# Kernel optimization log

Measured on AMD Instinct MI355X. Metric: run time of the kernel, lower is better.

The kernel has to match this reference:

```python
import jax, jax.numpy as jnp
import numpy as np
from jax import lax


def _dense_image_warp(img, flow):
    # TFA semantics: out[b,i,j] = bilinear_sample(img[b], (i - flow[b,i,j,0], j - flow[b,i,j,1]))
    # floors clamped to [0, size-2]; alphas clamped to [0, 1].
    B, H, W, C = img.shape
    gy = jnp.arange(H, dtype=flow.dtype)[None, :, None]
    gx = jnp.arange(W, dtype=flow.dtype)[None, None, :]
    qy = gy - flow[..., 0]
    qx = gx - flow[..., 1]
    fy = jnp.clip(jnp.floor(qy), 0.0, H - 2)
    fx = jnp.clip(jnp.floor(qx), 0.0, W - 2)
    ay = jnp.clip(qy - fy, 0.0, 1.0)[..., None]
    ax = jnp.clip(qx - fx, 0.0, 1.0)[..., None]
    fy = fy.astype(jnp.int32)
    fx = fx.astype(jnp.int32)
    b = jnp.arange(B)[:, None, None]
    tl = img[b, fy, fx]
    tr = img[b, fy, fx + 1]
    bl = img[b, fy + 1, fx]
    br = img[b, fy + 1, fx + 1]
    top = tl + ax * (tr - tl)
    bot = bl + ax * (br - bl)
    return top + ay * (bot - top)


def _conv(x, w, b, act):
    y = lax.conv_general_dilated(x, w, (1, 1), 'SAME',
                                 dimension_numbers=('NHWC', 'HWIO', 'NHWC')) + b
    return jax.nn.relu(y) if act else y


def _predict(x, ws, bs):
    for i in range(4):
        x = _conv(x, ws[i], bs[i], True)
    return _conv(x, ws[4], bs[4], False)  # final 1x1 -> 2 channels, linear


def _upsample2x(x):
    B, H, W, C = x.shape
    return jax.image.resize(x, (B, 2 * H, 2 * W, C), method='bilinear')


# Conv stack dims: in=64 (concat of two 32-ch maps)
_KSHAPES = [(3, 3, 64, 32), (3, 3, 32, 64), (1, 1, 64, 64), (1, 1, 64, 16), (1, 1, 16, 2)]


def setup_inputs() -> dict:
    key = jax.random.key(0)
    ks = jax.random.split(key, 4 + 2 * len(_KSHAPES))
    B, H, W, C = 8, 256, 256, 32
    inp = {
        'input_1': jax.random.normal(ks[0], (B, H, W, C), jnp.float32),
        'input_2': jax.random.normal(ks[1], (B, H, W, C), jnp.float32),
        'flow_1_2': jax.random.normal(ks[2], (B, H, W, 2), jnp.float32) * 3.0,
        'flow_2_1': jax.random.normal(ks[3], (B, H, W, 2), jnp.float32) * 3.0,
    }
    for i, sh in enumerate(_KSHAPES):
        inp[f'w12_{i}'] = jax.random.normal(ks[4 + i], sh, jnp.float32) * 0.05
        inp[f'b12_{i}'] = jnp.zeros((sh[-1],), jnp.float32)
        inp[f'w21_{i}'] = jax.random.normal(ks[4 + len(_KSHAPES) + i], sh, jnp.float32) * 0.05
        inp[f'b21_{i}'] = jnp.zeros((sh[-1],), jnp.float32)
    return inp


def reference(input_1, input_2, flow_1_2, flow_2_1,
              w12_0, b12_0, w12_1, b12_1, w12_2, b12_2, w12_3, b12_3, w12_4, b12_4,
              w21_0, b21_0, w21_1, b21_1, w21_2, b21_2, w21_3, b21_3, w21_4, b21_4):
    ws12 = [w12_0, w12_1, w12_2, w12_3, w12_4]
    bs12 = [b12_0, b12_1, b12_2, b12_3, b12_4]
    ws21 = [w21_0, w21_1, w21_2, w21_3, w21_4]
    bs21 = [b21_0, b21_1, b21_2, b21_3, b21_4]

    # 1 -> 2 direction
    input_1_warped_1 = _dense_image_warp(input_1, flow_1_2)
    flow_change_1_2 = _predict(jnp.concatenate([input_2, input_1_warped_1], axis=3), ws12, bs12)
    flow_1_2_changed = flow_1_2 + flow_change_1_2
    input_1_warped_2 = _dense_image_warp(input_1, flow_1_2_changed)
    flow_1_2_up = _upsample2x(flow_1_2_changed)

    # 2 -> 1 direction
    input_2_warped_1 = _dense_image_warp(input_2, flow_2_1)
    flow_change_2_1 = _predict(jnp.concatenate([input_1, input_2_warped_1], axis=3), ws21, bs21)
    flow_2_1_changed = flow_2_1 + flow_change_2_1
    input_2_warped_2 = _dense_image_warp(input_2, flow_2_1_changed)
    flow_2_1_up = _upsample2x(flow_2_1_changed)

    return (input_1_warped_2, input_2_warped_2, flow_1_2_up, flow_2_1_up)
```

## Files before the change

### kernel.cpp

```cpp
#include <hip/hip_runtime.h>
#include <hip/hip_bf16.h>
#include <cstddef>

#define B_ 8
#define H_ 256
#define W_ 256

static constexpr int NPIX = B_ * H_ * W_;

typedef __attribute__((ext_vector_type(8))) short bf16x8;
typedef __attribute__((ext_vector_type(4))) float f32x4;

__device__ __forceinline__ float4 ld4(const float* p) { return *(const float4*)p; }

__device__ __forceinline__ short f2bf(float x) {
    unsigned u = __float_as_uint(x);
    unsigned r = (u + 0x7fffu + ((u >> 16) & 1u)) >> 16;
    return (short)r;
}

__global__ __launch_bounds__(256) void cvt_inputs_kernel(
    const float* __restrict__ in1, const float* __restrict__ in2,
    short* __restrict__ xb1, short* __restrict__ xb2)
{
    int t = blockIdx.x * 256 + threadIdx.x;
    const int N8 = NPIX * 32 / 8;
    const float* src = (t < N8) ? in1 : in2;
    short* dst = (t < N8) ? xb1 : xb2;
    int i = (t < N8) ? t : t - N8;
    float4 a = ld4(src + (size_t)i * 8);
    float4 b = ld4(src + (size_t)i * 8 + 4);
    bf16x8 r;
    r[0] = f2bf(a.x); r[1] = f2bf(a.y); r[2] = f2bf(a.z); r[3] = f2bf(a.w);
    r[4] = f2bf(b.x); r[5] = f2bf(b.y); r[6] = f2bf(b.z); r[7] = f2bf(b.w);
    *(bf16x8*)(dst + (size_t)i * 8) = r;
}

__global__ __launch_bounds__(256) void prep_weights_kernel(
    const float* __restrict__ w0a, const float* __restrict__ w1a,
    const float* __restrict__ w2a, const float* __restrict__ w3a,
    const float* __restrict__ w0b, const float* __restrict__ w1b,
    const float* __restrict__ w2b, const float* __restrict__ w3b,
    short* __restrict__ wt0, short* __restrict__ wt1)
{
    int t = blockIdx.x * 256 + threadIdx.x;
    if (t >= 2 * 5248) return;
    int dir = t / 5248;
    int r = t % 5248;
    const float* w0 = dir ? w0b : w0a;
    const float* w1 = dir ? w1b : w1a;
    const float* w2 = dir ? w2b : w2a;
    const float* w3 = dir ? w3b : w3a;
    short* wt = dir ? wt1 : wt0;
    bf16x8 v;
    if (r < 2304) {
        int l = r & 63, n = (r >> 6) & 1, c = (r >> 7) & 1, tp = r >> 8;
#pragma unroll
        for (int j = 0; j < 8; ++j) {
            int ci = c * 32 + 8 * (l >> 4) + j;
            int co = n * 16 + (l & 15);
            v[j] = f2bf(w0[(size_t)(tp * 64 + ci) * 32 + co]);
        }
    } else if (r < 4608) {
        int q = r - 2304;
        int l = q & 63, n = (q >> 6) & 3, tp = q >> 8;
#pragma unroll
        for (int j = 0; j < 8; ++j) {
            int ci = 8 * (l >> 4) + j;
            int co = n * 16 + (l & 15);
            v[j] = f2bf(w1[(size_t)(tp * 32 + ci) * 64 + co]);
        }
    } else if (r < 5120) {
        int q = r - 4608;
        int l = q & 63, n = (q >> 6) & 3, c = q >> 8;
#pragma unroll
        for (int j = 0; j < 8; ++j) {
            int k = 32 * c + 8 * (l >> 4) + j;
            int co = n * 16 + (l & 15);
            v[j] = f2bf(w2[(size_t)k * 64 + co]);
        }
    } else {
        int q = r - 5120;
        int l = q & 63, c = q >> 6;
#pragma unroll
        for (int j = 0; j < 8; ++j) {
            int k = 32 * c + 8 * (l >> 4) + j;
            v[j] = f2bf(w3[(size_t)k * 16 + (l & 15)]);
        }
    }
    *(bf16x8*)(wt + (size_t)r * 8) = v;
}

__global__ __launch_bounds__(256) void warp_bf16_kernel(
    const float* __restrict__ in1, const float* __restrict__ in2,
    const float* __restrict__ fl12, const float* __restrict__ fl21,
    short* __restrict__ wbf)
{
    int gid = blockIdx.x * 256 + threadIdx.x;
    int d   = (gid >= NPIX * 8);
    int g2  = gid - (d ? NPIX * 8 : 0);
    const float* img  = d ? in2 : in1;
    const float* flow = d ? fl21 : fl12;
    short* out = wbf + (size_t)d * NPIX * 32;

    int p   = g2 >> 3;
    int c4  = (g2 & 7) << 2;
    int b   = p >> 16;
    int i   = (p >> 8) & 255;
    int j   = p & 255;
    float2 f = *(const float2*)(flow + (size_t)p * 2);
    float qy = (float)i - f.x;
    float qx = (float)j - f.y;
    float fyf = fminf(fmaxf(floorf(qy), 0.0f), (float)(H_ - 2));
    float fxf = fminf(fmaxf(floorf(qx), 0.0f), (float)(W_ - 2));
    float ay = fminf(fmaxf(qy - fyf, 0.0f), 1.0f);
    float ax = fminf(fmaxf(qx - fxf, 0.0f), 1.0f);
    int fy = (int)fyf, fx = (int)fxf;
    const float* base = img + ((((size_t)b * H_ + fy) * W_ + fx) << 5) + c4;
    float4 tl = ld4(base);
    float4 tr = ld4(base + 32);
    float4 bl = ld4(base + W_ * 32);
    float4 br = ld4(base + W_ * 32 + 32);
    short4 r;
    { float t = tl.x + ax * (tr.x - tl.x); float u = bl.x + ax * (br.x - bl.x); r.x = f2bf(t + ay * (u - t)); }
    { float t = tl.y + ax * (tr.y - tl.y); float u = bl.y + ax * (br.y - bl.y); r.y = f2bf(t + ay * (u - t)); }
    { float t = tl.z + ax * (tr.z - tl.z); float u = bl.z + ax * (br.z - bl.z); r.z = f2bf(t + ay * (u - t)); }
    { float t = tl.w + ax * (tr.w - tl.w); float u = bl.w + ax * (br.w - bl.w); r.w = f2bf(t + ay * (u - t)); }
    *(short4*)(out + ((size_t)p << 5) + c4) = r;
}

__global__ __launch_bounds__(256) void warp_f32_kernel(
    const float* __restrict__ in1, const float* __restrict__ in2,
    const float* __restrict__ fcb, float* __restrict__ outf)
{
    int gid = blockIdx.x * 256 + threadIdx.x;
    int d   = (gid >= NPIX * 8);
    int g2  = gid - (d ? NPIX * 8 : 0);
    const float* img  = d ? in2 : in1;
    const float* flow = fcb + (size_t)d * NPIX * 2;
    float* out = outf + (size_t)d * NPIX * 32;

    int p   = g2 >> 3;
    int c4  = (g2 & 7) << 2;
    int b   = p >> 16;
    int i   = (p >> 8) & 255;
    int j   = p & 255;
    float2 f = *(const float2*)(flow + (size_t)p * 2);
    float qy = (float)i - f.x;
    float qx = (float)j - f.y;
    float fyf = fminf(fmaxf(floorf(qy), 0.0f), (float)(H_ - 2));
    float fxf = fminf(fmaxf(floorf(qx), 0.0f), (float)(W_ - 2));
    float ay = fminf(fmaxf(qy - fyf, 0.0f), 1.0f);
    float ax = fminf(fmaxf(qx - fxf, 0.0f), 1.0f);
    int fy = (int)fyf, fx = (int)fxf;
    const float* base = img + ((((size_t)b * H_ + fy) * W_ + fx) << 5) + c4;
    float4 tl = ld4(base);
    float4 tr = ld4(base + 32);
    float4 bl = ld4(base + W_ * 32);
    float4 br = ld4(base + W_ * 32 + 32);
    float4 r;
    { float t = tl.x + ax * (tr.x - tl.x); float u = bl.x + ax * (br.x - bl.x); r.x = t + ay * (u - t); }
    { float t = tl.y + ax * (tr.y - tl.y); float u = bl.y + ax * (br.y - bl.y); r.y = t + ay * (u - t); }
    { float t = tl.z + ax * (tr.z - tl.z); float u = bl.z + ax * (br.z - bl.z); r.z = t + ay * (u - t); }
    { float t = tl.w + ax * (tr.w - tl.w); float u = bl.w + ax * (br.w - bl.w); r.w = t + ay * (u - t); }
    *(float4*)(out + ((size_t)p << 5) + c4) = r;
}

__global__ __launch_bounds__(512) void conv0_mfma_kernel(
    const short* __restrict__ xb1, const short* __restrict__ xb2,
    const short* __restrict__ wbf,
    const short* __restrict__ wt0, const short* __restrict__ wt1,
    const float* __restrict__ b0a, const float* __restrict__ b0b,
    short* __restrict__ h0)
{
    __shared__ short swt[2304 * 8];
    int d   = blockIdx.x >> 11;
    int bid = blockIdx.x & 2047;
    const short* xoth = d ? xb1 : xb2;
    const short* xw   = wbf + (size_t)d * NPIX * 32;
    const short* wtab = d ? wt1 : wt0;
    const float* bias = d ? b0b : b0a;
    short* out = h0 + (size_t)d * NPIX * 32;

    int tid = threadIdx.x;
    for (int i = tid; i < 2304; i += 512)
        ((bf16x8*)swt)[i] = ((const bf16x8*)wtab)[i];
    __syncthreads();

    int wave = tid >> 6, lane = tid & 63;
    int l15 = lane & 15, g = lane >> 4;
    int prow = bid * 256;
    int y    = bid & 255;
    int t0   = prow + wave * 32;
    int xl0  = wave * 32 + l15;
    int xl1  = xl0 + 16;

    const short* a0p = xoth + ((size_t)(t0 + l15) << 5) + g * 8;
    const short* a1p = a0p + (16 << 5);
    const short* b0p = xw + ((size_t)(t0 + l15) << 5) + g * 8;
    const short* b1p = b0p + (16 << 5);
    const bf16x8* wfrag = (const bf16x8*)swt;

    float bv0 = bias[l15], bv1 = bias[16 + l15];
    f32x4 acc00 = {bv0, bv0, bv0, bv0};
    f32x4 acc01 = {bv1, bv1, bv1, bv1};
    f32x4 acc10 = {bv0, bv0, bv0, bv0};
    f32x4 acc11 = {bv1, bv1, bv1, bv1};
    const bf16x8 z8 = {0, 0, 0, 0, 0, 0, 0, 0};

#pragma unroll
    for (int dy = -1; dy <= 1; ++dy) {
        if ((unsigned)(y + dy) >= (unsigned)H_) continue;
#pragma unroll
        for (int dx = -1; dx <= 1; ++dx) {
            bool v0 = (unsigned)(xl0 + dx) < (unsigned)W_;
            bool v1 = (unsigned)(xl1 + dx) < (unsigned)W_;
            int off0 = (dy * W_ + (v0 ? dx : 0)) << 5;
            int off1 = (dy * W_ + (v1 ? dx : 0)) << 5;
            bf16x8 aA0 = *(const bf16x8*)(a0p + off0);
            bf16x8 aB0 = *(const bf16x8*)(b0p + off0);
            bf16x8 aA1 = *(const bf16x8*)(a1p + off1);
            bf16x8 aB1 = *(const bf16x8*)(b1p + off1);
            aA0 = v0 ? aA0 : z8;  aB0 = v0 ? aB0 : z8;
            aA1 = v1 ? aA1 : z8;  aB1 = v1 ? aB1 : z8;
            int t = (dy + 1) * 3 + (dx + 1);
            bf16x8 w0 = wfrag[(t * 4 + 0) * 64 + lane];
            bf16x8 w1 = wfrag[(t * 4 + 1) * 64 + lane];
            bf16x8 w2 = wfrag[(t * 4 + 2) * 64 + lane];
            bf16x8 w3 = wfrag[(t * 4 + 3) * 64 + lane];
            acc00 = __builtin_amdgcn_mfma_f32_16x16x32_bf16(aA0, w0, acc00, 0, 0, 0);
            acc01 = __builtin_amdgcn_mfma_f32_16x16x32_bf16(aA0, w1, acc01, 0, 0, 0);
            acc10 = __builtin_amdgcn_mfma_f32_16x16x32_bf16(aA1, w0, acc10, 0, 0, 0);
            acc11 = __builtin_amdgcn_mfma_f32_16x16x32_bf16(aA1, w1, acc11, 0, 0, 0);
            acc00 = __builtin_amdgcn_mfma_f32_16x16x32_bf16(aB0, w2, acc00, 0, 0, 0);
            acc01 = __builtin_amdgcn_mfma_f32_16x16x32_bf16(aB0, w3, acc01, 0, 0, 0);
            acc10 = __builtin_amdgcn_mfma_f32_16x16x32_bf16(aB1, w2, acc10, 0, 0, 0);
            acc11 = __builtin_amdgcn_mfma_f32_16x16x32_bf16(aB1, w3, acc11, 0, 0, 0);
        }
    }

#pragma unroll
    for (int r = 0; r < 4; ++r) {
        size_t r0 = (size_t)(t0 + g * 4 + r) << 5;
        size_t r1 = (size_t)(t0 + 16 + g * 4 + r) << 5;
        out[r0 + l15]      = f2bf(fmaxf(acc00[r], 0.f));
        out[r0 + 16 + l15] = f2bf(fmaxf(acc01[r], 0.f));
        out[r1 + l15]      = f2bf(fmaxf(acc10[r], 0.f));
        out[r1 + 16 + l15] = f2bf(fmaxf(acc11[r], 0.f));
    }
}

__global__ __launch_bounds__(512) void conv1_mfma_kernel(
    const short* __restrict__ h0,
    const short* __restrict__ wt0, const short* __restrict__ wt1,
    const float* __restrict__ b1a, const float* __restrict__ b1b,
    const float* __restrict__ b2a, const float* __restrict__ b2b,
    const float* __restrict__ b3a, const float* __restrict__ b3b,
    const float* __restrict__ w4a, const float* __restrict__ w4b,
    const float* __restrict__ b4a, const float* __restrict__ b4b,
    const float* __restrict__ fl12, const float* __restrict__ fl21,
    float* __restrict__ fcb)
{
    __shared__ short swt[2944 * 8];
    __shared__ __align__(16) short sx[8][2048];
    int d   = blockIdx.x >> 11;
    int bid = blockIdx.x & 2047;
    const short* hsrc = h0 + (size_t)d * NPIX * 32;
    const short* wtab = (d ? wt1 : wt0) + 2304 * 8;
    const float* b1 = d ? b1b : b1a;
    const float* b2 = d ? b2b : b2a;
    const float* b3 = d ? b3b : b3a;
    const float* w4 = d ? w4b : w4a;
    const float* b4 = d ? b4b : b4a;
    const float* flow = d ? fl21 : fl12;
    float* fc = fcb + (size_t)d * NPIX * 2;

    int tid = threadIdx.x;
    for (int i = tid; i < 2944; i += 512)
        ((bf16x8*)swt)[i] = ((const bf16x8*)wtab)[i];
    __syncthreads();

    int wave = tid >> 6, lane = tid & 63;
    int l15 = lane & 15, g = lane >> 4;
    int prow = bid * 256;
    int y    = bid & 255;
    int t0   = prow + wave * 32;
    int xl0  = wave * 32 + l15;
    int xl1  = xl0 + 16;

    const short* a0p = hsrc + ((size_t)(t0 + l15) << 5) + g * 8;
    const short* a1p = a0p + (16 << 5);
    const bf16x8* W1 = (const bf16x8*)swt;
    const bf16x8* W2 = (const bf16x8*)swt + 2304;
    const bf16x8* W3 = (const bf16x8*)swt + 2816;
    char* xb = (char*)&sx[wave][0];
    const bf16x8 z8 = {0, 0, 0, 0, 0, 0, 0, 0};

    f32x4 acc0[4], acc1[4];
#pragma unroll
    for (int n = 0; n < 4; ++n) {
        float b = b1[n * 16 + l15];
        acc0[n] = (f32x4){b, b, b, b};
        acc1[n] = (f32x4){b, b, b, b};
    }
#pragma unroll
    for (int dy = -1; dy <= 1; ++dy) {
        if ((unsigned)(y + dy) >= (unsigned)H_) continue;
#pragma unroll
        for (int dx = -1; dx <= 1; ++dx) {
            bool v0 = (unsigned)(xl0 + dx) < (unsigned)W_;
            bool v1 = (unsigned)(xl1 + dx) < (unsigned)W_;
            int off0 = (dy * W_ + (v0 ? dx : 0)) << 5;
            int off1 = (dy * W_ + (v1 ? dx : 0)) << 5;
            bf16x8 a0 = *(const bf16x8*)(a0p + off0);
            bf16x8 a1 = *(const bf16x8*)(a1p + off1);
            a0 = v0 ? a0 : z8;
            a1 = v1 ? a1 : z8;
            int t = (dy + 1) * 3 + (dx + 1);
#pragma unroll
            for (int n = 0; n < 4; ++n) {
                bf16x8 w = W1[(t * 4 + n) * 64 + lane];
                acc0[n] = __builtin_amdgcn_mfma_f32_16x16x32_bf16(a0, w, acc0[n], 0, 0, 0);
                acc1[n] = __builtin_amdgcn_mfma_f32_16x16x32_bf16(a1, w, acc1[n], 0, 0, 0);
            }
        }
    }
#pragma unroll
    for (int n = 0; n < 4; ++n)
#pragma unroll
        for (int r = 0; r < 4; ++r) {
            int row0 = g * 4 + r, ch = n * 16 + l15;
            int by0 = (row0 * 128 + ch * 2) ^ ((row0 & 7) << 4);
            int by1 = ((row0 + 16) * 128 + ch * 2) ^ ((row0 & 7) << 4);
            *(short*)(xb + by0) = f2bf(fmaxf(acc0[n][r], 0.f));
            *(short*)(xb + by1) = f2bf(fmaxf(acc1[n][r], 0.f));
        }

#pragma unroll
    for (int n = 0; n < 4; ++n) {
        float b = b2[n * 16 + l15];
        acc0[n] = (f32x4){b, b, b, b};
        acc1[n] = (f32x4){b, b, b, b};
    }
#pragma unroll
    for (int c = 0; c < 2; ++c) {
        int by0 = (l15 * 128 + (32 * c + 8 * g) * 2) ^ ((l15 & 7) << 4);
        int by1 = ((l15 + 16) * 128 + (32 * c + 8 * g) * 2) ^ ((l15 & 7) << 4);
        bf16x8 a0 = *(const bf16x8*)(xb + by0);
        bf16x8 a1 = *(const bf16x8*)(xb + by1);
#pragma unroll
        for (int n = 0; n < 4; ++n) {
            bf16x8 w = W2[(c * 4 + n) * 64 + lane];
            acc0[n] = __builtin_amdgcn_mfma_f32_16x16x32_bf16(a0, w, acc0[n], 0, 0, 0);
            acc1[n] = __builtin_amdgcn_mfma_f32_16x16x32_bf16(a1, w, acc1[n], 0, 0, 0);
        }
    }
#pragma unroll
    for (int n = 0; n < 4; ++n)
#pragma unroll
        for (int r = 0; r < 4; ++r) {
            int row0 = g * 4 + r, ch = n * 16 + l15;
            int by0 = (row0 * 128 + ch * 2) ^ ((row0 & 7) << 4);
            int by1 = ((row0 + 16) * 128 + ch * 2) ^ ((row0 & 7) << 4);
            *(short*)(xb + by0) = f2bf(fmaxf(acc0[n][r], 0.f));
            *(short*)(xb + by1) = f2bf(fmaxf(acc1[n][r], 0.f));
        }

    float b3v = b3[l15];
    f32x4 acc3a = {b3v, b3v, b3v, b3v};
    f32x4 acc3b = {b3v, b3v, b3v, b3v};
#pragma unroll
    for (int c = 0; c < 2; ++c) {
        int by0 = (l15 * 128 + (32 * c + 8 * g) * 2) ^ ((l15 & 7) << 4);
        int by1 = ((l15 + 16) * 128 + (32 * c + 8 * g) * 2) ^ ((l15 & 7) << 4);
        bf16x8 a0 = *(const bf16x8*)(xb + by0);
        bf16x8 a1 = *(const bf16x8*)(xb + by1);
        bf16x8 w = W3[c * 64 + lane];
        acc3a = __builtin_amdgcn_mfma_f32_16x16x32_bf16(a0, w, acc3a, 0, 0, 0);
        acc3b = __builtin_amdgcn_mfma_f32_16x16x32_bf16(a1, w, acc3b, 0, 0, 0);
    }

    float w40 = w4[l15 * 2 + 0], w41 = w4[l15 * 2 + 1];
    float bb0 = b4[0], bb1 = b4[1];
#pragma unroll
    for (int tt = 0; tt < 2; ++tt) {
        f32x4 a3 = tt ? acc3b : acc3a;
#pragma unroll
        for (int r = 0; r < 4; ++r) {
            float v = fmaxf(a3[r], 0.f);
            float s0 = v * w40, s1 = v * w41;
#pragma unroll
            for (int m = 1; m < 16; m <<= 1) {
                s0 += __shfl_xor(s0, m);
                s1 += __shfl_xor(s1, m);
            }
            if (l15 == 0) {
                int pr = t0 + tt * 16 + g * 4 + r;
                float2 fl = *(const float2*)(flow + (size_t)pr * 2);
                float2 o; o.x = fl.x + bb0 + s0; o.y = fl.y + bb1 + s1;
                *(float2*)(fc + (size_t)pr * 2) = o;
            }
        }
    }
}

__global__ __launch_bounds__(256) void upsample_kernel(
    const float* __restrict__ fcb, float* __restrict__ outup)
{
    int gid = blockIdx.x * 256 + threadIdx.x;
    const int NUP = B_ * 512 * 512;
    int d  = (gid >= NUP);
    int g2 = gid - (d ? NUP : 0);
    const float* fc = fcb + (size_t)d * NPIX * 2;
    float* out = outup + (size_t)d * NUP * 2;

    int b  = g2 >> 18;
    int oy = (g2 >> 9) & 511;
    int ox = g2 & 511;
    float iy = 0.5f * (float)oy - 0.25f;
    float ix = 0.5f * (float)ox - 0.25f;
    float y0f = floorf(iy), x0f = floorf(ix);
    float wy = iy - y0f, wx = ix - x0f;
    int y0 = min(max((int)y0f, 0), H_ - 1);
    int y1 = min(max((int)y0f + 1, 0), H_ - 1);
    int x0 = min(max((int)x0f, 0), W_ - 1);
    int x1 = min(max((int)x0f + 1, 0), W_ - 1);
    float2 v00 = *(const float2*)(fc + (((size_t)b * H_ + y0) * W_ + x0) * 2);
    float2 v01 = *(const float2*)(fc + (((size_t)b * H_ + y0) * W_ + x1) * 2);
    float2 v10 = *(const float2*)(fc + (((size_t)b * H_ + y1) * W_ + x0) * 2);
    float2 v11 = *(const float2*)(fc + (((size_t)b * H_ + y1) * W_ + x1) * 2);
    float2 r;
    { float t = v00.x + wx * (v01.x - v00.x); float u = v10.x + wx * (v11.x - v10.x); r.x = t + wy * (u - t); }
    { float t = v00.y + wx * (v01.y - v00.y); float u = v10.y + wx * (v11.y - v10.y); r.y = t + wy * (u - t); }
    *(float2*)(out + (size_t)g2 * 2) = r;
}

extern "C" void kernel_launch(void* const* d_in, const int* in_sizes, int n_in,
                              void* d_out, int out_size, void* d_ws, size_t ws_size,
                              hipStream_t stream)
{
    (void)in_sizes; (void)n_in; (void)out_size; (void)ws_size;
    const float* input1 = (const float*)d_in[0];
    const float* input2 = (const float*)d_in[1];
    const float* fl12 = (const float*)d_in[2];
    const float* fl21 = (const float*)d_in[3];
    char* wsb = (char*)d_ws;
    short* xb1  = (short*)(wsb);
    short* xb2  = (short*)(wsb + 33554432);
    short* wbf  = (short*)(wsb + 67108864);
    short* h0   = (short*)(wsb + 134217728);
    float* fcb  = (float*)(wsb + 201326592);
    short* wt0  = (short*)(wsb + 209715200);
    short* wt1  = (short*)(wsb + 209715200 + 5248 * 16);
    float* outf = (float*)d_out;
    float* outup = outf + (size_t)2 * NPIX * 32;

    cvt_inputs_kernel<<<NPIX * 64 / 8 / 256, 256, 0, stream>>>(input1, input2, xb1, xb2);
    prep_weights_kernel<<<(2 * 5248 + 255) / 256, 256, 0, stream>>>(
        (const float*)d_in[4],  (const float*)d_in[8],  (const float*)d_in[12], (const float*)d_in[16],
        (const float*)d_in[6],  (const float*)d_in[10], (const float*)d_in[14], (const float*)d_in[18],
        wt0, wt1);
    warp_bf16_kernel<<<2 * NPIX * 8 / 256, 256, 0, stream>>>(input1, input2, fl12, fl21, wbf);
    conv0_mfma_kernel<<<2 * NPIX / 256, 512, 0, stream>>>(
        xb1, xb2, wbf, wt0, wt1,
        (const float*)d_in[5], (const float*)d_in[7], h0);
    conv1_mfma_kernel<<<2 * NPIX / 256, 512, 0, stream>>>(
        h0, wt0, wt1,
        (const float*)d_in[9],  (const float*)d_in[11],
        (const float*)d_in[13], (const float*)d_in[15],
        (const float*)d_in[17], (const float*)d_in[19],
        (const float*)d_in[20], (const float*)d_in[22],
        (const float*)d_in[21], (const float*)d_in[23],
        fl12, fl21, fcb);
    warp_f32_kernel<<<2 * NPIX * 8 / 256, 256, 0, stream>>>(input1, input2, fcb, outf);
    upsample_kernel<<<2 * B_ * 512 * 512 / 256, 256, 0, stream>>>(fcb, outup);
}
```

Measured before the change: 593.2 us.

## Widen warp kernels to 8 channels, XCD-swizzle conv blocks, register-cache conv1 weights

Both warp kernels now have each thread handle 8 channels instead of 4, which halves the thread count and index math and allows wider stores. The conv0 and conv1 kernels remap block IDs so that neighbouring workgroups land on the same XCD, aiming for better L2 locality. conv1 keeps its layer-2 and layer-3 weights in registers loaded from global memory rather than LDS. It also processes the two 16-row halves one after the other, cutting LDS use per wave to raise occupancy, at the cost of higher register pressure.

```diff
diff --git a/kernel.cpp b/kernel.cpp
--- a/kernel.cpp
+++ b/kernel.cpp
@@ -97,14 +97,14 @@
     short* __restrict__ wbf)
 {
     int gid = blockIdx.x * 256 + threadIdx.x;
-    int d   = (gid >= NPIX * 8);
-    int g2  = gid - (d ? NPIX * 8 : 0);
+    int d   = (gid >= NPIX * 4);
+    int g2  = gid - (d ? NPIX * 4 : 0);
     const float* img  = d ? in2 : in1;
     const float* flow = d ? fl21 : fl12;
     short* out = wbf + (size_t)d * NPIX * 32;
 
-    int p   = g2 >> 3;
-    int c4  = (g2 & 7) << 2;
+    int p   = g2 >> 2;
+    int c8  = (g2 & 3) << 3;
     int b   = p >> 16;
     int i   = (p >> 8) & 255;
     int j   = p & 255;
@@ -116,17 +116,20 @@
     float ay = fminf(fmaxf(qy - fyf, 0.0f), 1.0f);
     float ax = fminf(fmaxf(qx - fxf, 0.0f), 1.0f);
     int fy = (int)fyf, fx = (int)fxf;
-    const float* base = img + ((((size_t)b * H_ + fy) * W_ + fx) << 5) + c4;
-    float4 tl = ld4(base);
-    float4 tr = ld4(base + 32);
-    float4 bl = ld4(base + W_ * 32);
-    float4 br = ld4(base + W_ * 32 + 32);
-    short4 r;
-    { float t = tl.x + ax * (tr.x - tl.x); float u = bl.x + ax * (br.x - bl.x); r.x = f2bf(t + ay * (u - t)); }
-    { float t = tl.y + ax * (tr.y - tl.y); float u = bl.y + ax * (br.y - bl.y); r.y = f2bf(t + ay * (u - t)); }
-    { float t = tl.z + ax * (tr.z - tl.z); float u = bl.z + ax * (br.z - bl.z); r.z = f2bf(t + ay * (u - t)); }
-    { float t = tl.w + ax * (tr.w - tl.w); float u = bl.w + ax * (br.w - bl.w); r.w = f2bf(t + ay * (u - t)); }
-    *(short4*)(out + ((size_t)p << 5) + c4) = r;
+    const float* base = img + ((((size_t)b * H_ + fy) * W_ + fx) << 5) + c8;
+    float4 tl0 = ld4(base),            tl1 = ld4(base + 4);
+    float4 tr0 = ld4(base + 32),       tr1 = ld4(base + 36);
+    float4 bl0 = ld4(base + W_ * 32),      bl1 = ld4(base + W_ * 32 + 4);
+    float4 br0 = ld4(base + W_ * 32 + 32), br1 = ld4(base + W_ * 32 + 36);
+    bf16x8 r;
+#define WRP(k, TL, TR, BL, BR, m) \
+    { float t = TL.m + ax * (TR.m - TL.m); float u = BL.m + ax * (BR.m - BL.m); r[k] = f2bf(t + ay * (u - t)); }
+    WRP(0, tl0, tr0, bl0, br0, x) WRP(1, tl0, tr0, bl0, br0, y)
+    WRP(2, tl0, tr0, bl0, br0, z) WRP(3, tl0, tr0, bl0, br0, w)
+    WRP(4, tl1, tr1, bl1, br1, x) WRP(5, tl1, tr1, bl1, br1, y)
+    WRP(6, tl1, tr1, bl1, br1, z) WRP(7, tl1, tr1, bl1, br1, w)
+#undef WRP
+    *(bf16x8*)(out + ((size_t)p << 5) + c8) = r;
 }
 
 __global__ __launch_bounds__(256) void warp_f32_kernel(
@@ -134,14 +137,14 @@
     const float* __restrict__ fcb, float* __restrict__ outf)
 {
     int gid = blockIdx.x * 256 + threadIdx.x;
-    int d   = (gid >= NPIX * 8);
-    int g2  = gid - (d ? NPIX * 8 : 0);
+    int d   = (gid >= NPIX * 4);
+    int g2  = gid - (d ? NPIX * 4 : 0);
     const float* img  = d ? in2 : in1;
     const float* flow = fcb + (size_t)d * NPIX * 2;
     float* out = outf + (size_t)d * NPIX * 32;
 
-    int p   = g2 >> 3;
-    int c4  = (g2 & 7) << 2;
+    int p   = g2 >> 2;
+    int c8  = (g2 & 3) << 3;
     int b   = p >> 16;
     int i   = (p >> 8) & 255;
     int j   = p & 255;
@@ -153,17 +156,26 @@
     float ay = fminf(fmaxf(qy - fyf, 0.0f), 1.0f);
     float ax = fminf(fmaxf(qx - fxf, 0.0f), 1.0f);
     int fy = (int)fyf, fx = (int)fxf;
-    const float* base = img + ((((size_t)b * H_ + fy) * W_ + fx) << 5) + c4;
-    float4 tl = ld4(base);
-    float4 tr = ld4(base + 32);
-    float4 bl = ld4(base + W_ * 32);
-    float4 br = ld4(base + W_ * 32 + 32);
-    float4 r;
-    { float t = tl.x + ax * (tr.x - tl.x); float u = bl.x + ax * (br.x - bl.x); r.x = t + ay * (u - t); }
-    { float t = tl.y + ax * (tr.y - tl.y); float u = bl.y + ax * (br.y - bl.y); r.y = t + ay * (u - t); }
-    { float t = tl.z + ax * (tr.z - tl.z); float u = bl.z + ax * (br.z - bl.z); r.z = t + ay * (u - t); }
-    { float t = tl.w + ax * (tr.w - tl.w); float u = bl.w + ax * (br.w - bl.w); r.w = t + ay * (u - t); }
-    *(float4*)(out + ((size_t)p << 5) + c4) = r;
+    const float* base = img + ((((size_t)b * H_ + fy) * W_ + fx) << 5) + c8;
+    float4 tl0 = ld4(base),            tl1 = ld4(base + 4);
+    float4 tr0 = ld4(base + 32),       tr1 = ld4(base + 36);
+    float4 bl0 = ld4(base + W_ * 32),      bl1 = ld4(base + W_ * 32 + 4);
+    float4 br0 = ld4(base + W_ * 32 + 32), br1 = ld4(base + W_ * 32 + 36);
+    float4 r0, r1;
+#define WRPF(D, k, TL, TR, BL, BR, m) \
+    { float t = TL.m + ax * (TR.m - TL.m); float u = BL.m + ax * (BR.m - BL.m); D.k = t + ay * (u - t); }
+    WRPF(r0, x, tl0, tr0, bl0, br0, x) WRPF(r0, y, tl0, tr0, bl0, br0, y)
+    WRPF(r0, z, tl0, tr0, bl0, br0, z) WRPF(r0, w, tl0, tr0, bl0, br0, w)
+    WRPF(r1, x, tl1, tr1, bl1, br1, x) WRPF(r1, y, tl1, tr1, bl1, br1, y)
+    WRPF(r1, z, tl1, tr1, bl1, br1, z) WRPF(r1, w, tl1, tr1, bl1, br1, w)
+#undef WRPF
+    float* o = out + ((size_t)p << 5) + c8;
+    *(float4*)o = r0;
+    *(float4*)(o + 4) = r1;
+}
+
+__device__ __forceinline__ int xcd_swz(int orig) {
+    return (orig & 7) * 512 + (orig >> 3);
 }
 
 __global__ __launch_bounds__(512) void conv0_mfma_kernel(
@@ -174,8 +186,9 @@
     short* __restrict__ h0)
 {
     __shared__ short swt[2304 * 8];
-    int d   = blockIdx.x >> 11;
-    int bid = blockIdx.x & 2047;
+    int wg  = xcd_swz(blockIdx.x);
+    int d   = wg >> 11;
+    int bid = wg & 2047;
     const short* xoth = d ? xb1 : xb2;
     const short* xw   = wbf + (size_t)d * NPIX * 32;
     const short* wtab = d ? wt1 : wt0;
@@ -261,10 +274,11 @@
     const float* __restrict__ fl12, const float* __restrict__ fl21,
     float* __restrict__ fcb)
 {
-    __shared__ short swt[2944 * 8];
-    __shared__ __align__(16) short sx[8][2048];
-    int d   = blockIdx.x >> 11;
-    int bid = blockIdx.x & 2047;
+    __shared__ short swt[2304 * 8];
+    __shared__ __align__(16) short sx[8][1024];
+    int wg  = xcd_swz(blockIdx.x);
+    int d   = wg >> 11;
+    int bid = wg & 2047;
     const short* hsrc = h0 + (size_t)d * NPIX * 32;
     const short* wtab = (d ? wt1 : wt0) + 2304 * 8;
     const float* b1 = d ? b1b : b1a;
@@ -276,7 +290,7 @@
     float* fc = fcb + (size_t)d * NPIX * 2;
 
     int tid = threadIdx.x;
-    for (int i = tid; i < 2944; i += 512)
+    for (int i = tid; i < 2304; i += 512)
         ((bf16x8*)swt)[i] = ((const bf16x8*)wtab)[i];
     __syncthreads();
 
@@ -291,8 +305,8 @@
     const short* a0p = hsrc + ((size_t)(t0 + l15) << 5) + g * 8;
     const short* a1p = a0p + (16 << 5);
     const bf16x8* W1 = (const bf16x8*)swt;
-    const bf16x8* W2 = (const bf16x8*)swt + 2304;
-    const bf16x8* W3 = (const bf16x8*)swt + 2816;
+    const bf16x8* W2g = (const bf16x8*)wtab + 2304;
+    const bf16x8* W3g = (const bf16x8*)wtab + 2816;
     char* xb = (char*)&sx[wave][0];
     const bf16x8 z8 = {0, 0, 0, 0, 0, 0, 0, 0};
 
@@ -325,66 +339,58 @@
             }
         }
     }
-#pragma unroll
-    for (int n = 0; n < 4; ++n)
-#pragma unroll
-        for (int r = 0; r < 4; ++r) {
-            int row0 = g * 4 + r, ch = n * 16 + l15;
-            int by0 = (row0 * 128 + ch * 2) ^ ((row0 & 7) << 4);
-            int by1 = ((row0 + 16) * 128 + ch * 2) ^ ((row0 & 7) << 4);
-            *(short*)(xb + by0) = f2bf(fmaxf(acc0[n][r], 0.f));
-            *(short*)(xb + by1) = f2bf(fmaxf(acc1[n][r], 0.f));
-        }
-
-#pragma unroll
-    for (int n = 0; n < 4; ++n) {
-        float b = b2[n * 16 + l15];
-        acc0[n] = (f32x4){b, b, b, b};
-        acc1[n] = (f32x4){b, b, b, b};
-    }
+
+    bf16x8 w2r[8], w3r[2];
 #pragma unroll
     for (int c = 0; c < 2; ++c) {
-        int by0 = (l15 * 128 + (32 * c + 8 * g) * 2) ^ ((l15 & 7) << 4);
-        int by1 = ((l15 + 16) * 128 + (32 * c + 8 * g) * 2) ^ ((l15 & 7) << 4);
-        bf16x8 a0 = *(const bf16x8*)(xb + by0);
-        bf16x8 a1 = *(const bf16x8*)(xb + by1);
-#pragma unroll
-        for (int n = 0; n < 4; ++n) {
-            bf16x8 w = W2[(c * 4 + n) * 64 + lane];
-            acc0[n] = __builtin_amdgcn_mfma_f32_16x16x32_bf16(a0, w, acc0[n], 0, 0, 0);
-            acc1[n] = __builtin_amdgcn_mfma_f32_16x16x32_bf16(a1, w, acc1[n], 0, 0, 0);
-        }
-    }
-#pragma unroll
-    for (int n = 0; n < 4; ++n)
-#pragma unroll
-        for (int r = 0; r < 4; ++r) {
-            int row0 = g * 4 + r, ch = n * 16 + l15;
-            int by0 = (row0 * 128 + ch * 2) ^ ((row0 & 7) << 4);
-            int by1 = ((row0 + 16) * 128 + ch * 2) ^ ((row0 & 7) << 4);
-            *(short*)(xb + by0) = f2bf(fmaxf(acc0[n][r], 0.f));
-            *(short*)(xb + by1) = f2bf(fmaxf(acc1[n][r], 0.f));
-        }
+#pragma unroll
+        for (int n = 0; n < 4; ++n)
+            w2r[c * 4 + n] = W2g[(c * 4 + n) * 64 + lane];
+        w3r[c] = W3g[c * 64 + lane];
+    }
 
     float b3v = b3[l15];
-    f32x4 acc3a = {b3v, b3v, b3v, b3v};
-    f32x4 acc3b = {b3v, b3v, b3v, b3v};
-#pragma unroll
-    for (int c = 0; c < 2; ++c) {
-        int by0 = (l15 * 128 + (32 * c + 8 * g) * 2) ^ ((l15 & 7) << 4);
-        int by1 = ((l15 + 16) * 128 + (32 * c + 8 * g) * 2) ^ ((l15 & 7) << 4);
-        bf16x8 a0 = *(const bf16x8*)(xb + by0);
-        bf16x8 a1 = *(const bf16x8*)(xb + by1);
-        bf16x8 w = W3[c * 64 + lane];
-        acc3a = __builtin_amdgcn_mfma_f32_16x16x32_bf16(a0, w, acc3a, 0, 0, 0);
-        acc3b = __builtin_amdgcn_mfma_f32_16x16x32_bf16(a1, w, acc3b, 0, 0, 0);
-    }
-
     float w40 = w4[l15 * 2 + 0], w41 = w4[l15 * 2 + 1];
     float bb0 = b4[0], bb1 = b4[1];
-#pragma unroll
-    for (int tt = 0; tt < 2; ++tt) {
-        f32x4 a3 = tt ? acc3b : acc3a;
+    float b2v[4];
+#pragma unroll
+    for (int n = 0; n < 4; ++n) b2v[n] = b2[n * 16 + l15];
+
+    auto tail = [&](f32x4 (&accT)[4], int tbase) {
+#pragma unroll
+        for (int n = 0; n < 4; ++n)
+#pragma unroll
+            for (int r = 0; r < 4; ++r) {
+                int row = g * 4 + r, ch = n * 16 + l15;
+                int by = (row * 128 + ch * 2) ^ ((row & 7) << 4);
+                *(short*)(xb + by) = f2bf(fmaxf(accT[n][r], 0.f));
+            }
+        f32x4 t2[4];
+#pragma unroll
+        for (int n = 0; n < 4; ++n) t2[n] = (f32x4){b2v[n], b2v[n], b2v[n], b2v[n]};
+#pragma unroll
+        for (int c = 0; c < 2; ++c) {
+            int by = (l15 * 128 + (32 * c + 8 * g) * 2) ^ ((l15 & 7) << 4);
+            bf16x8 a = *(const bf16x8*)(xb + by);
+#pragma unroll
+            for (int n = 0; n < 4; ++n)
+                t2[n] = __builtin_amdgcn_mfma_f32_16x16x32_bf16(a, w2r[c * 4 + n], t2[n], 0, 0, 0);
+        }
+#pragma unroll
+        for (int n = 0; n < 4; ++n)
+#pragma unroll
+            for (int r = 0; r < 4; ++r) {
+                int row = g * 4 + r, ch = n * 16 + l15;
+                int by = (row * 128 + ch * 2) ^ ((row & 7) << 4);
+                *(short*)(xb + by) = f2bf(fmaxf(t2[n][r], 0.f));
+            }
+        f32x4 a3 = {b3v, b3v, b3v, b3v};
+#pragma unroll
+        for (int c = 0; c < 2; ++c) {
+            int by = (l15 * 128 + (32 * c + 8 * g) * 2) ^ ((l15 & 7) << 4);
+            bf16x8 a = *(const bf16x8*)(xb + by);
+            a3 = __builtin_amdgcn_mfma_f32_16x16x32_bf16(a, w3r[c], a3, 0, 0, 0);
+        }
 #pragma unroll
         for (int r = 0; r < 4; ++r) {
             float v = fmaxf(a3[r], 0.f);
@@ -395,13 +401,15 @@
                 s1 += __shfl_xor(s1, m);
             }
             if (l15 == 0) {
-                int pr = t0 + tt * 16 + g * 4 + r;
+                int pr = tbase + g * 4 + r;
                 float2 fl = *(const float2*)(flow + (size_t)pr * 2);
                 float2 o; o.x = fl.x + bb0 + s0; o.y = fl.y + bb1 + s1;
                 *(float2*)(fc + (size_t)pr * 2) = o;
             }
         }
-    }
+    };
+    tail(acc0, t0);
+    tail(acc1, t0 + 16);
 }
 
 __global__ __launch_bounds__(256) void upsample_kernel(
@@ -460,7 +468,7 @@
         (const float*)d_in[4],  (const float*)d_in[8],  (const float*)d_in[12], (const float*)d_in[16],
         (const float*)d_in[6],  (const float*)d_in[10], (const float*)d_in[14], (const float*)d_in[18],
         wt0, wt1);
-    warp_bf16_kernel<<<2 * NPIX * 8 / 256, 256, 0, stream>>>(input1, input2, fl12, fl21, wbf);
+    warp_bf16_kernel<<<2 * NPIX * 4 / 256, 256, 0, stream>>>(input1, input2, fl12, fl21, wbf);
     conv0_mfma_kernel<<<2 * NPIX / 256, 512, 0, stream>>>(
         xb1, xb2, wbf, wt0, wt1,
         (const float*)d_in[5], (const float*)d_in[7], h0);
@@ -472,6 +480,6 @@
         (const float*)d_in[20], (const float*)d_in[22],
         (const float*)d_in[21], (const float*)d_in[23],
         fl12, fl21, fcb);
-    warp_f32_kernel<<<2 * NPIX * 8 / 256, 256, 0, stream>>>(input1, input2, fcb, outf);
+    warp_f32_kernel<<<2 * NPIX * 4 / 256, 256, 0, stream>>>(input1, input2, fcb, outf);
     upsample_kernel<<<2 * B_ * 512 * 512 / 256, 256, 0, stream>>>(fcb, outup);
 }
```

Result: slower. 647.6 us (+9.2%).
